# Kernel optimization log

Hardware: AMD Instinct MI355X
Metric: run time of the kernel (lower is better)

The kernel has to match this reference:

```python
import jax, jax.numpy as jnp
import numpy as np

N_NODES = 50000
N_EDGES = 800000
DIM_IN, DIM_H, DIM_OUT = 128, 128, 64


def _init_linear(key, fan_in, fan_out):
    # kaiming-uniform-ish init, matches torch Linear scale
    lim = 1.0 / np.sqrt(fan_in)
    return jax.random.uniform(key, (fan_in, fan_out), jnp.float32, -lim, lim)


def setup_inputs() -> dict:
    key = jax.random.key(0)
    ks = jax.random.split(key, 12)
    x = jax.random.normal(ks[0], (N_NODES, DIM_IN), jnp.float32)
    edge_index = jax.random.randint(ks[1], (2, N_EDGES), 0, N_NODES, jnp.int32)
    dims = [(DIM_IN, DIM_H), (DIM_H, DIM_H), (DIM_H, DIM_OUT)]
    inp = {"x": x, "edge_index": edge_index}
    for i, (fi, fo) in enumerate(dims):
        inp[f"Wl{i}"] = _init_linear(ks[2 + 3 * i], fi, fo)   # neighbor transform
        inp[f"Wr{i}"] = _init_linear(ks[3 + 3 * i], fi, fo)   # root transform
        inp[f"b{i}"] = jnp.zeros((fo,), jnp.float32)
    return inp


def _sage_layer(x, src, dst, Wl, Wr, b):
    # mean aggregation of neighbor messages x[src] at destination nodes
    msg = x[src]                                              # [E, d]
    agg = jax.ops.segment_sum(msg, dst, num_segments=N_NODES)  # [N, d]
    cnt = jax.ops.segment_sum(jnp.ones((src.shape[0],), x.dtype), dst,
                              num_segments=N_NODES)
    mean = agg / jnp.maximum(cnt, 1.0)[:, None]               # isolated nodes -> 0
    return mean @ Wl + b + x @ Wr                              # SAGEConv


def reference(x, edge_index, Wl0, Wr0, b0, Wl1, Wr1, b1, Wl2, Wr2, b2):
    src, dst = edge_index[0], edge_index[1]
    layers = [(Wl0, Wr0, b0), (Wl1, Wr1, b1), (Wl2, Wr2, b2)]
    h = x
    for i, (Wl, Wr, b) in enumerate(layers):
        h = _sage_layer(h, src, dst, Wl, Wr, b)
        if i != len(layers) - 1:
            h = jax.nn.relu(h)  # dropout p=0.2 is identity in eval mode
    return jax.nn.log_softmax(h, axis=1), h
```

## Files before the change

### kernel.cpp

```cpp
#include <hip/hip_runtime.h>

#define N_NODES 50000
#define N_EDGES 800000
#define SCAN_BLOCKS 196
#define WIN 6250

typedef __attribute__((ext_vector_type(8))) short short8;
typedef __attribute__((ext_vector_type(4))) float f32x4;
typedef unsigned short ushort_t;
typedef unsigned int uint_t;

__device__ inline ushort_t f2bf(float f) {
    union { float f; uint_t u; } v; v.f = f;
    uint_t u = v.u;
    u += 0x7fffu + ((u >> 16) & 1u);
    return (ushort_t)(u >> 16);
}
__device__ inline float bflo(uint_t v) { return __uint_as_float(v << 16); }
__device__ inline float bfhi(uint_t v) { return __uint_as_float(v & 0xffff0000u); }
__device__ inline float bf2f(ushort_t v) { return __uint_as_float((uint_t)v << 16); }

#define ACC8(V) { a[0] += bflo((V).x); a[1] += bfhi((V).x); \
                  a[2] += bflo((V).y); a[3] += bfhi((V).y); \
                  a[4] += bflo((V).z); a[5] += bfhi((V).z); \
                  a[6] += bflo((V).w); a[7] += bfhi((V).w); }

__global__ void prep(const int* __restrict__ ei, int* __restrict__ cnt,
                     const float* __restrict__ x, ushort_t* __restrict__ x_bf,
                     const float* __restrict__ Wl0, const float* __restrict__ Wr0,
                     const float* __restrict__ Wl1, const float* __restrict__ Wr1,
                     const float* __restrict__ Wl2, const float* __restrict__ Wr2,
                     ushort_t* __restrict__ pk0, ushort_t* __restrict__ pk1,
                     ushort_t* __restrict__ pkz) {
    int b = blockIdx.x;
    if (b < 1024) {
        int g = b & 7;
        int bi = b >> 3;
        int lo = g * WIN;
        const int4* dv = (const int4*)(ei + N_EDGES);
        for (int q = bi * 256 + threadIdx.x; q < N_EDGES / 4; q += 128 * 256) {
            int4 d = dv[q];
            if ((unsigned)(d.x - lo) < WIN) atomicAdd(&cnt[d.x], 1);
            if ((unsigned)(d.y - lo) < WIN) atomicAdd(&cnt[d.y], 1);
            if ((unsigned)(d.z - lo) < WIN) atomicAdd(&cnt[d.z], 1);
            if ((unsigned)(d.w - lo) < WIN) atomicAdd(&cnt[d.w], 1);
        }
    } else if (b < 7274) {
        int i = (b - 1024) * 256 + threadIdx.x;
        if (i < 1600000) {
            float4 v = ((const float4*)x)[i];
            ushort4 o;
            o.x = f2bf(v.x); o.y = f2bf(v.y); o.z = f2bf(v.z); o.w = f2bf(v.w);
            ((ushort4*)x_bf)[i] = o;
        }
    } else {
        int gi = (b - 7274) * 256 + threadIdx.x;
        const float* Wl; const float* Wr; ushort_t* dst; int idx; bool zr = false;
        if (gi < 32768)       { Wl = Wl0; Wr = Wr0; dst = pk0; idx = gi; }
        else if (gi < 65536)  { Wl = Wl1; Wr = Wr1; dst = pk1; idx = gi - 32768; }
        else if (gi < 81920)  { Wl = Wl2; Wr = Wr2; dst = pkz; idx = gi - 65536; zr = true; }
        else return;
        int j = idx & 7, l = (idx >> 3) & 63, t = (idx >> 9) & 7, ks = idx >> 12;
        int n = t * 16 + (l & 15);
        int k = ks * 32 + (l >> 4) * 8 + j;
        float w;
        if (zr) w = (n < 64) ? Wl[k * 64 + n] : Wr[k * 64 + (n - 64)];
        else    w = (k < 128) ? Wl[k * 128 + n] : Wr[(k - 128) * 128 + n];
        dst[idx] = f2bf(w);
    }
}

__global__ void fill_csr_mp(const int* __restrict__ ei, int* __restrict__ cursor,
                            int* __restrict__ csr_src) {
    int g = blockIdx.x & 7;
    int nb = gridDim.x >> 3;
    int bi = blockIdx.x >> 3;
    int lo = g * WIN;
    const int4* dv = (const int4*)(ei + N_EDGES);
    const int4* sv = (const int4*)ei;
    for (int q = bi * 256 + threadIdx.x; q < N_EDGES / 4; q += nb * 256) {
        int4 d = dv[q];
        bool m0 = (unsigned)(d.x - lo) < WIN;
        bool m1 = (unsigned)(d.y - lo) < WIN;
        bool m2 = (unsigned)(d.z - lo) < WIN;
        bool m3 = (unsigned)(d.w - lo) < WIN;
        if (m0 | m1 | m2 | m3) {
            int4 s = sv[q];
            if (m0) { int p = atomicAdd(&cursor[d.x], 1); csr_src[p] = s.x; }
            if (m1) { int p = atomicAdd(&cursor[d.y], 1); csr_src[p] = s.y; }
            if (m2) { int p = atomicAdd(&cursor[d.z], 1); csr_src[p] = s.z; }
            if (m3) { int p = atomicAdd(&cursor[d.w], 1); csr_src[p] = s.w; }
        }
    }
}

__global__ void block_sums(const int* __restrict__ cnt, int* __restrict__ bsum) {
    int i = blockIdx.x * 256 + threadIdx.x;
    int v = (i < N_NODES) ? cnt[i] : 0;
    for (int off = 32; off; off >>= 1) v += __shfl_down(v, off, 64);
    __shared__ int s[4];
    if ((threadIdx.x & 63) == 0) s[threadIdx.x >> 6] = v;
    __syncthreads();
    if (threadIdx.x == 0) bsum[blockIdx.x] = s[0] + s[1] + s[2] + s[3];
}

__global__ void apply_scan2(const int* __restrict__ cnt, const int* __restrict__ bsum,
                            int* __restrict__ rowstart, int* __restrict__ cursor) {
    __shared__ int s[256];
    __shared__ int p[256];
    int t = threadIdx.x;
    int i = blockIdx.x * 256 + t;
    int v = (i < N_NODES) ? cnt[i] : 0;
    int bv = (t < SCAN_BLOCKS) ? bsum[t] : 0;
    s[t] = v;
    p[t] = bv;
    __syncthreads();
    for (int off = 1; off < 256; off <<= 1) {
        int as_ = (t >= off) ? s[t - off] : 0;
        int ap_ = (t >= off) ? p[t - off] : 0;
        __syncthreads();
        s[t] += as_;
        p[t] += ap_;
        __syncthreads();
    }
    int bprefix = (blockIdx.x > 0) ? p[blockIdx.x - 1] : 0;
    int excl = s[t] - v + bprefix;
    if (i < N_NODES) { rowstart[i] = excl; cursor[i] = excl; }
    if (blockIdx.x == 0 && t == 0) rowstart[N_NODES] = N_EDGES;
}

template <bool ZR>
__global__ __launch_bounds__(256) void sage_fused_k(
    const ushort_t* __restrict__ feat_bf,
    const int* __restrict__ rowstart,
    const int* __restrict__ csr_src,
    const ushort_t* __restrict__ Bpk, const float* __restrict__ bias,
    const ushort_t* __restrict__ Bz, const float* __restrict__ bias2,
    ushort_t* __restrict__ out_bf,
    ushort_t* __restrict__ z_bf, float* __restrict__ r_f32) {
    __shared__ uint_t mlds[64][68];
    int lane = threadIdx.x & 63;
    int wave = threadIdx.x >> 6;
    int rowBase = blockIdx.x * 64 + wave * 16;
    int sub = lane >> 4;
    int sl  = lane & 15;
    int gb  = sub << 4;
    const uint_t* base = (const uint_t*)feat_bf;

    for (int p = 0; p < 4; ++p) {
        int node = rowBase + p * 4 + sub;
        int s0 = 0, s1 = 0;
        if (node < N_NODES) { s0 = rowstart[node]; s1 = rowstart[node + 1]; }
        float a[8];
        #pragma unroll
        for (int k = 0; k < 8; ++k) a[k] = 0.f;

        int pos = s0;
        while (__any(pos < s1)) {
            int m = min(16, s1 - pos);
            int idxr = (sl < m) ? csr_src[pos + sl] : 0;
            int mm = max(m, 0);
            mm = max(mm, __shfl_xor(mm, 16, 64));
            mm = max(mm, __shfl_xor(mm, 32, 64));
            for (int j = 0; j < mm; j += 8) {
                int  sidx[8];
                bool vld[8];
                #pragma unroll
                for (int k = 0; k < 8; ++k) {
                    int q = __shfl(idxr, (gb + j + k) & 63, 64);
                    vld[k]  = (j + k < m);
                    sidx[k] = vld[k] ? q : 0;
                }
                uint4 V[8];
                #pragma unroll
                for (int k = 0; k < 8; ++k)
                    V[k] = *(const uint4*)(base + (size_t)sidx[k] * 64 + (sl << 2));
                #pragma unroll
                for (int k = 0; k < 8; ++k)
                    if (vld[k]) { ACC8(V[k]); }
            }
            pos += 16;
        }
        float inv = 1.0f / fmaxf((float)(s1 - s0), 1.0f);
        uint4 o;
        o.x = (uint_t)f2bf(a[0] * inv) | ((uint_t)f2bf(a[1] * inv) << 16);
        o.y = (uint_t)f2bf(a[2] * inv) | ((uint_t)f2bf(a[3] * inv) << 16);
        o.z = (uint_t)f2bf(a[4] * inv) | ((uint_t)f2bf(a[5] * inv) << 16);
        o.w = (uint_t)f2bf(a[6] * inv) | ((uint_t)f2bf(a[7] * inv) << 16);
        *((uint4*)&mlds[wave * 16 + p * 4 + sub][sl << 2]) = o;
    }
    __syncthreads();

    int row16 = lane & 15;
    int quad  = lane >> 4;
    int arow  = min(rowBase + row16, N_NODES - 1);
    const ushort_t* rrow = feat_bf + (size_t)arow * 128;
    const short8* bp = (const short8*)Bpk + lane;

    f32x4 acc[8];
    #pragma unroll
    for (int t = 0; t < 8; ++t) { f32x4 z = {0.f, 0.f, 0.f, 0.f}; acc[t] = z; }

    #pragma unroll
    for (int ks = 0; ks < 8; ++ks) {
        short8 afrag;
        if (ks < 4)
            afrag = *(const short8*)&mlds[wave * 16 + row16][ks * 16 + quad * 4];
        else
            afrag = *(const short8*)(rrow + (ks - 4) * 32 + quad * 8);
        #pragma unroll
        for (int t = 0; t < 8; ++t) {
            short8 bfrag = bp[(ks * 8 + t) * 64];
            acc[t] = __builtin_amdgcn_mfma_f32_16x16x32_bf16(afrag, bfrag, acc[t], 0, 0, 0);
        }
    }

    if (!ZR) {
        #pragma unroll
        for (int t = 0; t < 8; ++t) {
            int col = t * 16 + row16;
            float bv = bias[col];
            #pragma unroll
            for (int r = 0; r < 4; ++r) {
                int row = rowBase + quad * 4 + r;
                if (row < N_NODES) {
                    float v = fmaxf(acc[t][r] + bv, 0.f);
                    out_bf[(size_t)row * 128 + col] = f2bf(v);
                }
            }
        }
    } else {
        #pragma unroll
        for (int t = 0; t < 8; ++t) {
            int col = t * 16 + row16;
            float bv = bias[col];
            #pragma unroll
            for (int r = 0; r < 4; ++r) {
                float v = fmaxf(acc[t][r] + bv, 0.f);
                ((ushort_t*)&mlds[wave * 16 + quad * 4 + r][0])[col] = f2bf(v);
            }
        }
        __syncthreads();

        const short8* bz = (const short8*)Bz + lane;
        f32x4 acc2[8];
        #pragma unroll
        for (int t = 0; t < 8; ++t) { f32x4 z = {0.f, 0.f, 0.f, 0.f}; acc2[t] = z; }

        #pragma unroll
        for (int ks = 0; ks < 4; ++ks) {
            short8 afrag = *(const short8*)((const ushort_t*)&mlds[wave * 16 + row16][0]
                                            + ks * 32 + quad * 8);
            #pragma unroll
            for (int t = 0; t < 8; ++t) {
                short8 bfrag = bz[(ks * 8 + t) * 64];
                acc2[t] = __builtin_amdgcn_mfma_f32_16x16x32_bf16(afrag, bfrag, acc2[t], 0, 0, 0);
            }
        }

        #pragma unroll
        for (int t = 0; t < 8; ++t) {
            int col = t * 16 + row16;
            #pragma unroll
            for (int r = 0; r < 4; ++r) {
                int row = rowBase + quad * 4 + r;
                if (row < N_NODES) {
                    if (col < 64) {
                        z_bf[(size_t)row * 64 + col] = f2bf(acc2[t][r]);
                    } else {
                        r_f32[(size_t)row * 64 + (col - 64)] = acc2[t][r] + bias2[col - 64];
                    }
                }
            }
        }
    }
}

__global__ __launch_bounds__(256) void final_agg_softmax2(
    const ushort_t* __restrict__ z_bf, const float* __restrict__ r_f32,
    const int* __restrict__ rowstart, const int* __restrict__ csr_src,
    float* __restrict__ out) {
    int lane = threadIdx.x & 63;
    int wave = threadIdx.x >> 6;
    int sub = lane >> 3;
    int sl  = lane & 7;
    int gb  = sub << 3;
    int node = blockIdx.x * 32 + wave * 8 + sub;
    int s0 = 0, s1 = 0;
    if (node < N_NODES) { s0 = rowstart[node]; s1 = rowstart[node + 1]; }

    float a[8];
    #pragma unroll
    for (int k = 0; k < 8; ++k) a[k] = 0.f;
    const uint_t* zb = (const uint_t*)z_bf;

    int pos = s0;
    while (__any(pos < s1)) {
        int m = min(8, s1 - pos);
        int idxr = (sl < m) ? csr_src[pos + sl] : 0;
        int  sidx[8];
        bool vld[8];
        #pragma unroll
        for (int k = 0; k < 8; ++k) {
            int q = __shfl(idxr, (gb + k) & 63, 64);
            vld[k]  = (k < m);
            sidx[k] = vld[k] ? q : 0;
        }
        uint4 V[8];
        #pragma unroll
        for (int k = 0; k < 8; ++k)
            V[k] = *(const uint4*)(zb + (size_t)sidx[k] * 32 + (sl << 2));
        #pragma unroll
        for (int k = 0; k < 8; ++k)
            if (vld[k]) { ACC8(V[k]); }
        pos += 8;
    }
    if (node >= N_NODES) return;

    float inv = 1.0f / fmaxf((float)(s1 - s0), 1.0f);
    const float4* rr = (const float4*)(r_f32 + (size_t)node * 64 + sl * 8);
    float4 rA = rr[0], rB = rr[1];
    float h[8];
    h[0] = a[0] * inv + rA.x; h[1] = a[1] * inv + rA.y;
    h[2] = a[2] * inv + rA.z; h[3] = a[3] * inv + rA.w;
    h[4] = a[4] * inv + rB.x; h[5] = a[5] * inv + rB.y;
    h[6] = a[6] * inv + rB.z; h[7] = a[7] * inv + rB.w;

    float mx = fmaxf(fmaxf(fmaxf(h[0], h[1]), fmaxf(h[2], h[3])),
                     fmaxf(fmaxf(h[4], h[5]), fmaxf(h[6], h[7])));
    mx = fmaxf(mx, __shfl_xor(mx, 1, 64));
    mx = fmaxf(mx, __shfl_xor(mx, 2, 64));
    mx = fmaxf(mx, __shfl_xor(mx, 4, 64));
    float s = 0.f;
    #pragma unroll
    for (int k = 0; k < 8; ++k) s += expf(h[k] - mx);
    s += __shfl_xor(s, 1, 64);
    s += __shfl_xor(s, 2, 64);
    s += __shfl_xor(s, 4, 64);
    float lse = mx + logf(s);

    size_t o1 = (size_t)node * 64 + sl * 8;
    size_t o2 = (size_t)N_NODES * 64 + o1;
    *(float4*)(out + o1)     = make_float4(h[0] - lse, h[1] - lse, h[2] - lse, h[3] - lse);
    *(float4*)(out + o1 + 4) = make_float4(h[4] - lse, h[5] - lse, h[6] - lse, h[7] - lse);
    *(float4*)(out + o2)     = make_float4(h[0], h[1], h[2], h[3]);
    *(float4*)(out + o2 + 4) = make_float4(h[4], h[5], h[6], h[7]);
}

extern "C" void kernel_launch(void* const* d_in, const int* in_sizes, int n_in,
                              void* d_out, int out_size, void* d_ws, size_t ws_size,
                              hipStream_t stream) {
    const float* x  = (const float*)d_in[0];
    const int* ei   = (const int*)d_in[1];
    const float* Wl0 = (const float*)d_in[2];
    const float* Wr0 = (const float*)d_in[3];
    const float* b0  = (const float*)d_in[4];
    const float* Wl1 = (const float*)d_in[5];
    const float* Wr1 = (const float*)d_in[6];
    const float* b1  = (const float*)d_in[7];
    const float* Wl2 = (const float*)d_in[8];
    const float* Wr2 = (const float*)d_in[9];
    const float* b2  = (const float*)d_in[10];
    float* out = (float*)d_out;

    char* ws = (char*)d_ws;
    int* cnt      = (int*)(ws + 0x000000);
    int* rowstart = (int*)(ws + 0x040000);
    int* cursor   = (int*)(ws + 0x080000);
    int* bsum     = (int*)(ws + 0x0C0000);
    int* csr_src  = (int*)(ws + 0x100000);
    ushort_t* pk0 = (ushort_t*)(ws + 0x420000);
    ushort_t* pk1 = (ushort_t*)(ws + 0x440000);
    ushort_t* pkz = (ushort_t*)(ws + 0x460000);
    ushort_t* x_bf = (ushort_t*)(ws + 0x0500000);
    ushort_t* h_bf = (ushort_t*)(ws + 0x1200000);
    ushort_t* z_bf = (ushort_t*)(ws + 0x1F00000);
    float*    r_f32 = (float*)  (ws + 0x2600000);

    hipMemsetAsync(cnt, 0, N_NODES * sizeof(int), stream);
    prep<<<7594, 256, 0, stream>>>(ei, cnt, x, x_bf,
                                   Wl0, Wr0, Wl1, Wr1, Wl2, Wr2, pk0, pk1, pkz);

    block_sums<<<SCAN_BLOCKS, 256, 0, stream>>>(cnt, bsum);
    apply_scan2<<<SCAN_BLOCKS, 256, 0, stream>>>(cnt, bsum, rowstart, cursor);
    fill_csr_mp<<<1024, 256, 0, stream>>>(ei, cursor, csr_src);

    sage_fused_k<false><<<782, 256, 0, stream>>>(x_bf, rowstart, csr_src, pk0, b0,
                                                 nullptr, nullptr, h_bf, nullptr, nullptr);

    sage_fused_k<true><<<782, 256, 0, stream>>>(h_bf, rowstart, csr_src, pk1, b1,
                                                pkz, b2, nullptr, z_bf, r_f32);

    final_agg_softmax2<<<1563, 256, 0, stream>>>(z_bf, r_f32, rowstart, csr_src, out);
}
```

Before: 275.1 us.

## Fuse whole GNN pipeline into one cooperative persistent kernel with grid syncs

Replaces the chain of seven launches plus a memset with a single cooperative kernel of 782 blocks. Phases (conversion, degree count, scan, CSR fill, two SAGE layers, final aggregation and softmax) are separated by grid.sync. The aim is to remove launch gaps and tail drain between stages. In exchange, the grid is much smaller for the conversion and counting phases, and each grid barrier has its own cost. The old multi-kernel path stays as a fallback if the cooperative launch fails.

```diff
diff --git a/kernel.cpp b/kernel.cpp
--- a/kernel.cpp
+++ b/kernel.cpp
@@ -1,9 +1,13 @@
 #include <hip/hip_runtime.h>
+#include <hip/hip_cooperative_groups.h>
+
+namespace cg = cooperative_groups;
 
 #define N_NODES 50000
 #define N_EDGES 800000
 #define SCAN_BLOCKS 196
 #define WIN 6250
+#define GRID_ALL 782
 
 typedef __attribute__((ext_vector_type(8))) short short8;
 typedef __attribute__((ext_vector_type(4))) float f32x4;
@@ -18,119 +22,15 @@
 }
 __device__ inline float bflo(uint_t v) { return __uint_as_float(v << 16); }
 __device__ inline float bfhi(uint_t v) { return __uint_as_float(v & 0xffff0000u); }
-__device__ inline float bf2f(ushort_t v) { return __uint_as_float((uint_t)v << 16); }
 
 #define ACC8(V) { a[0] += bflo((V).x); a[1] += bfhi((V).x); \
                   a[2] += bflo((V).y); a[3] += bfhi((V).y); \
                   a[4] += bflo((V).z); a[5] += bfhi((V).z); \
                   a[6] += bflo((V).w); a[7] += bfhi((V).w); }
 
-__global__ void prep(const int* __restrict__ ei, int* __restrict__ cnt,
-                     const float* __restrict__ x, ushort_t* __restrict__ x_bf,
-                     const float* __restrict__ Wl0, const float* __restrict__ Wr0,
-                     const float* __restrict__ Wl1, const float* __restrict__ Wr1,
-                     const float* __restrict__ Wl2, const float* __restrict__ Wr2,
-                     ushort_t* __restrict__ pk0, ushort_t* __restrict__ pk1,
-                     ushort_t* __restrict__ pkz) {
-    int b = blockIdx.x;
-    if (b < 1024) {
-        int g = b & 7;
-        int bi = b >> 3;
-        int lo = g * WIN;
-        const int4* dv = (const int4*)(ei + N_EDGES);
-        for (int q = bi * 256 + threadIdx.x; q < N_EDGES / 4; q += 128 * 256) {
-            int4 d = dv[q];
-            if ((unsigned)(d.x - lo) < WIN) atomicAdd(&cnt[d.x], 1);
-            if ((unsigned)(d.y - lo) < WIN) atomicAdd(&cnt[d.y], 1);
-            if ((unsigned)(d.z - lo) < WIN) atomicAdd(&cnt[d.z], 1);
-            if ((unsigned)(d.w - lo) < WIN) atomicAdd(&cnt[d.w], 1);
-        }
-    } else if (b < 7274) {
-        int i = (b - 1024) * 256 + threadIdx.x;
-        if (i < 1600000) {
-            float4 v = ((const float4*)x)[i];
-            ushort4 o;
-            o.x = f2bf(v.x); o.y = f2bf(v.y); o.z = f2bf(v.z); o.w = f2bf(v.w);
-            ((ushort4*)x_bf)[i] = o;
-        }
-    } else {
-        int gi = (b - 7274) * 256 + threadIdx.x;
-        const float* Wl; const float* Wr; ushort_t* dst; int idx; bool zr = false;
-        if (gi < 32768)       { Wl = Wl0; Wr = Wr0; dst = pk0; idx = gi; }
-        else if (gi < 65536)  { Wl = Wl1; Wr = Wr1; dst = pk1; idx = gi - 32768; }
-        else if (gi < 81920)  { Wl = Wl2; Wr = Wr2; dst = pkz; idx = gi - 65536; zr = true; }
-        else return;
-        int j = idx & 7, l = (idx >> 3) & 63, t = (idx >> 9) & 7, ks = idx >> 12;
-        int n = t * 16 + (l & 15);
-        int k = ks * 32 + (l >> 4) * 8 + j;
-        float w;
-        if (zr) w = (n < 64) ? Wl[k * 64 + n] : Wr[k * 64 + (n - 64)];
-        else    w = (k < 128) ? Wl[k * 128 + n] : Wr[(k - 128) * 128 + n];
-        dst[idx] = f2bf(w);
-    }
-}
-
-__global__ void fill_csr_mp(const int* __restrict__ ei, int* __restrict__ cursor,
-                            int* __restrict__ csr_src) {
-    int g = blockIdx.x & 7;
-    int nb = gridDim.x >> 3;
-    int bi = blockIdx.x >> 3;
-    int lo = g * WIN;
-    const int4* dv = (const int4*)(ei + N_EDGES);
-    const int4* sv = (const int4*)ei;
-    for (int q = bi * 256 + threadIdx.x; q < N_EDGES / 4; q += nb * 256) {
-        int4 d = dv[q];
-        bool m0 = (unsigned)(d.x - lo) < WIN;
-        bool m1 = (unsigned)(d.y - lo) < WIN;
-        bool m2 = (unsigned)(d.z - lo) < WIN;
-        bool m3 = (unsigned)(d.w - lo) < WIN;
-        if (m0 | m1 | m2 | m3) {
-            int4 s = sv[q];
-            if (m0) { int p = atomicAdd(&cursor[d.x], 1); csr_src[p] = s.x; }
-            if (m1) { int p = atomicAdd(&cursor[d.y], 1); csr_src[p] = s.y; }
-            if (m2) { int p = atomicAdd(&cursor[d.z], 1); csr_src[p] = s.z; }
-            if (m3) { int p = atomicAdd(&cursor[d.w], 1); csr_src[p] = s.w; }
-        }
-    }
-}
-
-__global__ void block_sums(const int* __restrict__ cnt, int* __restrict__ bsum) {
-    int i = blockIdx.x * 256 + threadIdx.x;
-    int v = (i < N_NODES) ? cnt[i] : 0;
-    for (int off = 32; off; off >>= 1) v += __shfl_down(v, off, 64);
-    __shared__ int s[4];
-    if ((threadIdx.x & 63) == 0) s[threadIdx.x >> 6] = v;
-    __syncthreads();
-    if (threadIdx.x == 0) bsum[blockIdx.x] = s[0] + s[1] + s[2] + s[3];
-}
-
-__global__ void apply_scan2(const int* __restrict__ cnt, const int* __restrict__ bsum,
-                            int* __restrict__ rowstart, int* __restrict__ cursor) {
-    __shared__ int s[256];
-    __shared__ int p[256];
-    int t = threadIdx.x;
-    int i = blockIdx.x * 256 + t;
-    int v = (i < N_NODES) ? cnt[i] : 0;
-    int bv = (t < SCAN_BLOCKS) ? bsum[t] : 0;
-    s[t] = v;
-    p[t] = bv;
-    __syncthreads();
-    for (int off = 1; off < 256; off <<= 1) {
-        int as_ = (t >= off) ? s[t - off] : 0;
-        int ap_ = (t >= off) ? p[t - off] : 0;
-        __syncthreads();
-        s[t] += as_;
-        p[t] += ap_;
-        __syncthreads();
-    }
-    int bprefix = (blockIdx.x > 0) ? p[blockIdx.x - 1] : 0;
-    int excl = s[t] - v + bprefix;
-    if (i < N_NODES) { rowstart[i] = excl; cursor[i] = excl; }
-    if (blockIdx.x == 0 && t == 0) rowstart[N_NODES] = N_EDGES;
-}
-
 template <bool ZR>
-__global__ __launch_bounds__(256) void sage_fused_k(
+__device__ __forceinline__ void layer_phase(
+    uint_t (*mlds)[68],
     const ushort_t* __restrict__ feat_bf,
     const int* __restrict__ rowstart,
     const int* __restrict__ csr_src,
@@ -138,7 +38,6 @@
     const ushort_t* __restrict__ Bz, const float* __restrict__ bias2,
     ushort_t* __restrict__ out_bf,
     ushort_t* __restrict__ z_bf, float* __restrict__ r_f32) {
-    __shared__ uint_t mlds[64][68];
     int lane = threadIdx.x & 63;
     int wave = threadIdx.x >> 6;
     int rowBase = blockIdx.x * 64 + wave * 16;
@@ -276,7 +175,8 @@
     }
 }
 
-__global__ __launch_bounds__(256) void final_agg_softmax2(
+__device__ __forceinline__ void final_phase_vb(
+    int vb,
     const ushort_t* __restrict__ z_bf, const float* __restrict__ r_f32,
     const int* __restrict__ rowstart, const int* __restrict__ csr_src,
     float* __restrict__ out) {
@@ -285,7 +185,7 @@
     int sub = lane >> 3;
     int sl  = lane & 7;
     int gb  = sub << 3;
-    int node = blockIdx.x * 32 + wave * 8 + sub;
+    int node = vb * 32 + wave * 8 + sub;
     int s0 = 0, s1 = 0;
     if (node < N_NODES) { s0 = rowstart[node]; s1 = rowstart[node + 1]; }
 
@@ -345,6 +245,256 @@
     *(float4*)(out + o1 + 4) = make_float4(h[4] - lse, h[5] - lse, h[6] - lse, h[7] - lse);
     *(float4*)(out + o2)     = make_float4(h[0], h[1], h[2], h[3]);
     *(float4*)(out + o2 + 4) = make_float4(h[4], h[5], h[6], h[7]);
+}
+
+__global__ __launch_bounds__(256, 4) void sage_all(
+    const float* __restrict__ x, const int* __restrict__ ei,
+    const float* __restrict__ Wl0, const float* __restrict__ Wr0, const float* __restrict__ b0,
+    const float* __restrict__ Wl1, const float* __restrict__ Wr1, const float* __restrict__ b1,
+    const float* __restrict__ Wl2, const float* __restrict__ Wr2, const float* __restrict__ b2,
+    int* __restrict__ cnt, int* __restrict__ rowstart, int* __restrict__ cursor,
+    int* __restrict__ bsum, int* __restrict__ csr_src,
+    ushort_t* __restrict__ pk0, ushort_t* __restrict__ pk1, ushort_t* __restrict__ pkz,
+    ushort_t* __restrict__ x_bf, ushort_t* __restrict__ h_bf,
+    ushort_t* __restrict__ z_bf, float* __restrict__ r_f32,
+    float* __restrict__ out) {
+    cg::grid_group grid = cg::this_grid();
+    __shared__ uint_t mlds[64][68];
+    __shared__ int ssc[256];
+    __shared__ int psc[256];
+    __shared__ int s4[4];
+
+    const int tid = blockIdx.x * 256 + threadIdx.x;
+    const int nthr = gridDim.x * 256;
+
+    for (int i = tid; i < N_NODES; i += nthr) cnt[i] = 0;
+    for (int i = tid; i < 1600000; i += nthr) {
+        float4 v = ((const float4*)x)[i];
+        ushort4 o;
+        o.x = f2bf(v.x); o.y = f2bf(v.y); o.z = f2bf(v.z); o.w = f2bf(v.w);
+        ((ushort4*)x_bf)[i] = o;
+    }
+    for (int gi = tid; gi < 81920; gi += nthr) {
+        const float* Wl; const float* Wr; ushort_t* dst; int idx; bool zr = false;
+        if (gi < 32768)      { Wl = Wl0; Wr = Wr0; dst = pk0; idx = gi; }
+        else if (gi < 65536) { Wl = Wl1; Wr = Wr1; dst = pk1; idx = gi - 32768; }
+        else                 { Wl = Wl2; Wr = Wr2; dst = pkz; idx = gi - 65536; zr = true; }
+        int j = idx & 7, l = (idx >> 3) & 63, t = (idx >> 9) & 7, ks = idx >> 12;
+        int n = t * 16 + (l & 15);
+        int k = ks * 32 + (l >> 4) * 8 + j;
+        float w;
+        if (zr) w = (n < 64) ? Wl[k * 64 + n] : Wr[k * 64 + (n - 64)];
+        else    w = (k < 128) ? Wl[k * 128 + n] : Wr[(k - 128) * 128 + n];
+        dst[idx] = f2bf(w);
+    }
+    grid.sync();
+
+    {
+        int role = blockIdx.x & 7, bi = blockIdx.x >> 3;
+        int nbr = (gridDim.x + 7 - role) >> 3;
+        int lo = role * WIN;
+        const int4* dv = (const int4*)(ei + N_EDGES);
+        for (int q = bi * 256 + threadIdx.x; q < N_EDGES / 4; q += nbr * 256) {
+            int4 d = dv[q];
+            if ((unsigned)(d.x - lo) < WIN) atomicAdd(&cnt[d.x], 1);
+            if ((unsigned)(d.y - lo) < WIN) atomicAdd(&cnt[d.y], 1);
+            if ((unsigned)(d.z - lo) < WIN) atomicAdd(&cnt[d.z], 1);
+            if ((unsigned)(d.w - lo) < WIN) atomicAdd(&cnt[d.w], 1);
+        }
+    }
+    grid.sync();
+
+    if (blockIdx.x < SCAN_BLOCKS) {
+        int i = blockIdx.x * 256 + threadIdx.x;
+        int v = (i < N_NODES) ? cnt[i] : 0;
+        for (int off = 32; off; off >>= 1) v += __shfl_down(v, off, 64);
+        if ((threadIdx.x & 63) == 0) s4[threadIdx.x >> 6] = v;
+        __syncthreads();
+        if (threadIdx.x == 0) bsum[blockIdx.x] = s4[0] + s4[1] + s4[2] + s4[3];
+    }
+    grid.sync();
+
+    if (blockIdx.x < SCAN_BLOCKS) {
+        int t = threadIdx.x;
+        int i = blockIdx.x * 256 + t;
+        int v = (i < N_NODES) ? cnt[i] : 0;
+        int bv = (t < SCAN_BLOCKS) ? bsum[t] : 0;
+        ssc[t] = v;
+        psc[t] = bv;
+        __syncthreads();
+        for (int off = 1; off < 256; off <<= 1) {
+            int as_ = (t >= off) ? ssc[t - off] : 0;
+            int ap_ = (t >= off) ? psc[t - off] : 0;
+            __syncthreads();
+            ssc[t] += as_;
+            psc[t] += ap_;
+            __syncthreads();
+        }
+        int bprefix = (blockIdx.x > 0) ? psc[blockIdx.x - 1] : 0;
+        int excl = ssc[t] - v + bprefix;
+        if (i < N_NODES) { rowstart[i] = excl; cursor[i] = excl; }
+        if (blockIdx.x == 0 && t == 0) rowstart[N_NODES] = N_EDGES;
+    }
+    grid.sync();
+
+    {
+        int role = blockIdx.x & 7, bi = blockIdx.x >> 3;
+        int nbr = (gridDim.x + 7 - role) >> 3;
+        int lo = role * WIN;
+        const int4* dv = (const int4*)(ei + N_EDGES);
+        const int4* sv = (const int4*)ei;
+        for (int q = bi * 256 + threadIdx.x; q < N_EDGES / 4; q += nbr * 256) {
+            int4 d = dv[q];
+            bool m0 = (unsigned)(d.x - lo) < WIN;
+            bool m1 = (unsigned)(d.y - lo) < WIN;
+            bool m2 = (unsigned)(d.z - lo) < WIN;
+            bool m3 = (unsigned)(d.w - lo) < WIN;
+            if (m0 | m1 | m2 | m3) {
+                int4 s = sv[q];
+                if (m0) { int p = atomicAdd(&cursor[d.x], 1); csr_src[p] = s.x; }
+                if (m1) { int p = atomicAdd(&cursor[d.y], 1); csr_src[p] = s.y; }
+                if (m2) { int p = atomicAdd(&cursor[d.z], 1); csr_src[p] = s.z; }
+                if (m3) { int p = atomicAdd(&cursor[d.w], 1); csr_src[p] = s.w; }
+            }
+        }
+    }
+    grid.sync();
+
+    layer_phase<false>(mlds, x_bf, rowstart, csr_src, pk0, b0,
+                       nullptr, nullptr, h_bf, nullptr, nullptr);
+    grid.sync();
+
+    layer_phase<true>(mlds, h_bf, rowstart, csr_src, pk1, b1,
+                      pkz, b2, nullptr, z_bf, r_f32);
+    grid.sync();
+
+    for (int vb = blockIdx.x; vb < 1563; vb += gridDim.x)
+        final_phase_vb(vb, z_bf, r_f32, rowstart, csr_src, out);
+}
+
+__global__ void prep(const int* __restrict__ ei, int* __restrict__ cnt,
+                     const float* __restrict__ x, ushort_t* __restrict__ x_bf,
+                     const float* __restrict__ Wl0, const float* __restrict__ Wr0,
+                     const float* __restrict__ Wl1, const float* __restrict__ Wr1,
+                     const float* __restrict__ Wl2, const float* __restrict__ Wr2,
+                     ushort_t* __restrict__ pk0, ushort_t* __restrict__ pk1,
+                     ushort_t* __restrict__ pkz) {
+    int b = blockIdx.x;
+    if (b < 1024) {
+        int g = b & 7;
+        int bi = b >> 3;
+        int lo = g * WIN;
+        const int4* dv = (const int4*)(ei + N_EDGES);
+        for (int q = bi * 256 + threadIdx.x; q < N_EDGES / 4; q += 128 * 256) {
+            int4 d = dv[q];
+            if ((unsigned)(d.x - lo) < WIN) atomicAdd(&cnt[d.x], 1);
+            if ((unsigned)(d.y - lo) < WIN) atomicAdd(&cnt[d.y], 1);
+            if ((unsigned)(d.z - lo) < WIN) atomicAdd(&cnt[d.z], 1);
+            if ((unsigned)(d.w - lo) < WIN) atomicAdd(&cnt[d.w], 1);
+        }
+    } else if (b < 7274) {
+        int i = (b - 1024) * 256 + threadIdx.x;
+        if (i < 1600000) {
+            float4 v = ((const float4*)x)[i];
+            ushort4 o;
+            o.x = f2bf(v.x); o.y = f2bf(v.y); o.z = f2bf(v.z); o.w = f2bf(v.w);
+            ((ushort4*)x_bf)[i] = o;
+        }
+    } else {
+        int gi = (b - 7274) * 256 + threadIdx.x;
+        const float* Wl; const float* Wr; ushort_t* dst; int idx; bool zr = false;
+        if (gi < 32768)       { Wl = Wl0; Wr = Wr0; dst = pk0; idx = gi; }
+        else if (gi < 65536)  { Wl = Wl1; Wr = Wr1; dst = pk1; idx = gi - 32768; }
+        else if (gi < 81920)  { Wl = Wl2; Wr = Wr2; dst = pkz; idx = gi - 65536; zr = true; }
+        else return;
+        int j = idx & 7, l = (idx >> 3) & 63, t = (idx >> 9) & 7, ks = idx >> 12;
+        int n = t * 16 + (l & 15);
+        int k = ks * 32 + (l >> 4) * 8 + j;
+        float w;
+        if (zr) w = (n < 64) ? Wl[k * 64 + n] : Wr[k * 64 + (n - 64)];
+        else    w = (k < 128) ? Wl[k * 128 + n] : Wr[(k - 128) * 128 + n];
+        dst[idx] = f2bf(w);
+    }
+}
+
+__global__ void fill_csr_mp(const int* __restrict__ ei, int* __restrict__ cursor,
+                            int* __restrict__ csr_src) {
+    int g = blockIdx.x & 7;
+    int nb = gridDim.x >> 3;
+    int bi = blockIdx.x >> 3;
+    int lo = g * WIN;
+    const int4* dv = (const int4*)(ei + N_EDGES);
+    const int4* sv = (const int4*)ei;
+    for (int q = bi * 256 + threadIdx.x; q < N_EDGES / 4; q += nb * 256) {
+        int4 d = dv[q];
+        bool m0 = (unsigned)(d.x - lo) < WIN;
+        bool m1 = (unsigned)(d.y - lo) < WIN;
+        bool m2 = (unsigned)(d.z - lo) < WIN;
+        bool m3 = (unsigned)(d.w - lo) < WIN;
+        if (m0 | m1 | m2 | m3) {
+            int4 s = sv[q];
+            if (m0) { int p = atomicAdd(&cursor[d.x], 1); csr_src[p] = s.x; }
+            if (m1) { int p = atomicAdd(&cursor[d.y], 1); csr_src[p] = s.y; }
+            if (m2) { int p = atomicAdd(&cursor[d.z], 1); csr_src[p] = s.z; }
+            if (m3) { int p = atomicAdd(&cursor[d.w], 1); csr_src[p] = s.w; }
+        }
+    }
+}
+
+__global__ void block_sums(const int* __restrict__ cnt, int* __restrict__ bsum) {
+    int i = blockIdx.x * 256 + threadIdx.x;
+    int v = (i < N_NODES) ? cnt[i] : 0;
+    for (int off = 32; off; off >>= 1) v += __shfl_down(v, off, 64);
+    __shared__ int s[4];
+    if ((threadIdx.x & 63) == 0) s[threadIdx.x >> 6] = v;
+    __syncthreads();
+    if (threadIdx.x == 0) bsum[blockIdx.x] = s[0] + s[1] + s[2] + s[3];
+}
+
+__global__ void apply_scan2(const int* __restrict__ cnt, const int* __restrict__ bsum,
+                            int* __restrict__ rowstart, int* __restrict__ cursor) {
+    __shared__ int s[256];
+    __shared__ int p[256];
+    int t = threadIdx.x;
+    int i = blockIdx.x * 256 + t;
+    int v = (i < N_NODES) ? cnt[i] : 0;
+    int bv = (t < SCAN_BLOCKS) ? bsum[t] : 0;
+    s[t] = v;
+    p[t] = bv;
+    __syncthreads();
+    for (int off = 1; off < 256; off <<= 1) {
+        int as_ = (t >= off) ? s[t - off] : 0;
+        int ap_ = (t >= off) ? p[t - off] : 0;
+        __syncthreads();
+        s[t] += as_;
+        p[t] += ap_;
+        __syncthreads();
+    }
+    int bprefix = (blockIdx.x > 0) ? p[blockIdx.x - 1] : 0;
+    int excl = s[t] - v + bprefix;
+    if (i < N_NODES) { rowstart[i] = excl; cursor[i] = excl; }
+    if (blockIdx.x == 0 && t == 0) rowstart[N_NODES] = N_EDGES;
+}
+
+template <bool ZR>
+__global__ __launch_bounds__(256) void sage_fused_k(
+    const ushort_t* __restrict__ feat_bf,
+    const int* __restrict__ rowstart,
+    const int* __restrict__ csr_src,
+    const ushort_t* __restrict__ Bpk, const float* __restrict__ bias,
+    const ushort_t* __restrict__ Bz, const float* __restrict__ bias2,
+    ushort_t* __restrict__ out_bf,
+    ushort_t* __restrict__ z_bf, float* __restrict__ r_f32) {
+    __shared__ uint_t mlds[64][68];
+    layer_phase<ZR>(mlds, feat_bf, rowstart, csr_src, Bpk, bias, Bz, bias2,
+                    out_bf, z_bf, r_f32);
+}
+
+__global__ __launch_bounds__(256) void final_agg_softmax2(
+    const ushort_t* __restrict__ z_bf, const float* __restrict__ r_f32,
+    const int* __restrict__ rowstart, const int* __restrict__ csr_src,
+    float* __restrict__ out) {
+    final_phase_vb(blockIdx.x, z_bf, r_f32, rowstart, csr_src, out);
 }
 
 extern "C" void kernel_launch(void* const* d_in, const int* in_sizes, int n_in,
@@ -377,19 +527,29 @@
     ushort_t* z_bf = (ushort_t*)(ws + 0x1F00000);
     float*    r_f32 = (float*)  (ws + 0x2600000);
 
+    void* kargs[] = {
+        (void*)&x, (void*)&ei,
+        (void*)&Wl0, (void*)&Wr0, (void*)&b0,
+        (void*)&Wl1, (void*)&Wr1, (void*)&b1,
+        (void*)&Wl2, (void*)&Wr2, (void*)&b2,
+        (void*)&cnt, (void*)&rowstart, (void*)&cursor, (void*)&bsum, (void*)&csr_src,
+        (void*)&pk0, (void*)&pk1, (void*)&pkz,
+        (void*)&x_bf, (void*)&h_bf, (void*)&z_bf, (void*)&r_f32,
+        (void*)&out
+    };
+    hipError_t err = hipLaunchCooperativeKernel((void*)sage_all, dim3(GRID_ALL),
+                                                dim3(256), kargs, 0, stream);
+    if (err == hipSuccess) return;
+
     hipMemsetAsync(cnt, 0, N_NODES * sizeof(int), stream);
     prep<<<7594, 256, 0, stream>>>(ei, cnt, x, x_bf,
                                    Wl0, Wr0, Wl1, Wr1, Wl2, Wr2, pk0, pk1, pkz);
-
     block_sums<<<SCAN_BLOCKS, 256, 0, stream>>>(cnt, bsum);
     apply_scan2<<<SCAN_BLOCKS, 256, 0, stream>>>(cnt, bsum, rowstart, cursor);
     fill_csr_mp<<<1024, 256, 0, stream>>>(ei, cursor, csr_src);
-
     sage_fused_k<false><<<782, 256, 0, stream>>>(x_bf, rowstart, csr_src, pk0, b0,
                                                  nullptr, nullptr, h_bf, nullptr, nullptr);
-
     sage_fused_k<true><<<782, 256, 0, stream>>>(h_bf, rowstart, csr_src, pk1, b1,
                                                 pkz, b2, nullptr, z_bf, r_f32);
-
     final_agg_softmax2<<<1563, 256, 0, stream>>>(z_bf, r_f32, rowstart, csr_src, out);
 }
```

Result: slower. 940.2 us (+241.8%).
